# Kernel tuning notes

Hardware: AMD Instinct MI355X
Metric: run time of the kernel (lower is better)

## Reference

```python
import jax, jax.numpy as jnp
import numpy as np

NUM_EXPERTS = 8
HIDDEN = 2048
INTER = 4096
TOKENS = 8192
TOP_K = 2


def setup_inputs() -> dict:
    key = jax.random.key(0)
    ks = jax.random.split(key, 5)
    s = 0.02
    return {
        "x": jax.random.normal(ks[0], (TOKENS, HIDDEN), dtype=jnp.float32),
        "gate_w": jax.random.normal(ks[1], (NUM_EXPERTS, HIDDEN), dtype=jnp.float32) * s,
        "w1": jax.random.normal(ks[2], (NUM_EXPERTS, INTER, HIDDEN), dtype=jnp.float32) * s,
        "w2": jax.random.normal(ks[3], (NUM_EXPERTS, HIDDEN, INTER), dtype=jnp.float32) * s,
        "w3": jax.random.normal(ks[4], (NUM_EXPERTS, INTER, HIDDEN), dtype=jnp.float32) * s,
    }


def reference(x, gate_w, w1, w2, w3):
    # Router: softmax over experts in fp32, then top-2 (no renormalization,
    # matching the torch module which uses the raw top-k softmax probs).
    router_logits = jnp.einsum("th,eh->te", x, gate_w)  # [T, E]
    probs = jax.nn.softmax(router_logits.astype(jnp.float32), axis=1)
    topk_w, topk_idx = jax.lax.top_k(probs, TOP_K)  # [T, K]
    topk_w = topk_w.astype(x.dtype)

    num_experts = w1.shape[0]
    out = jnp.zeros_like(x)
    for e in range(num_experts):
        # Combined routing coefficient for expert e per token (0 if unrouted).
        coef = jnp.sum(jnp.where(topk_idx == e, topk_w, 0.0), axis=1)  # [T]
        # SwiGLU expert FFN: down(silu(gate(x)) * up(x))
        g = jnp.einsum("th,ih->ti", x, w1[e])
        u = jnp.einsum("th,ih->ti", x, w3[e])
        h = jax.nn.silu(g) * u
        y = jnp.einsum("ti,hi->th", h, w2[e])
        out = out + coef[:, None] * y
    return out
```

## Files before the change

### kernel.cpp

```cpp
#include <hip/hip_runtime.h>
#include <stdint.h>
#include <stddef.h>


constexpr int kTokens  = 8192;
constexpr int kHidden  = 2048;
constexpr int kInter   = 4096;
constexpr int kExperts = 8;

constexpr int BM = 128, BN = 128, BK = 64;
constexpr int MAX_MT = (2 * kTokens) / BM + kExperts;
constexpr int NTY = kInter / BK;
constexpr int NPAN_Y5 = kHidden / 256;
constexpr int kSlotCap = 16512;

typedef short bf16x8 __attribute__((ext_vector_type(8)));
typedef float f32x4  __attribute__((ext_vector_type(4)));
typedef unsigned int u32;

__device__ __forceinline__ unsigned short f2bf(float f) {
  union { float f; unsigned u; } v; v.f = f;
  unsigned r = v.u + 0x7FFFu + ((v.u >> 16) & 1u);
  return (unsigned short)(r >> 16);
}

__device__ __forceinline__ void gload16(const void* g, void* l) {
  __builtin_amdgcn_global_load_lds(
      (const __attribute__((address_space(1))) u32*)g,
      (__attribute__((address_space(3))) u32*)l, 16, 0, 0);
}

__global__ __launch_bounds__(256) void convert_w(
    const float* __restrict__ src, unsigned short* __restrict__ dst,
    int lp, int lq, int K, long nchunks)
{
  long stride = (long)gridDim.x * blockDim.x;
  for (long g = blockIdx.x * (long)blockDim.x + threadIdx.x; g < nchunks; g += stride) {
    int  l   = (int)(g & 1023);
    long blk = g >> 10;
    int  q   = (int)(blk & ((1 << lq) - 1));
    long ep  = blk >> lq;
    int  p   = (int)(ep & ((1 << lp) - 1));
    int  e   = (int)(ep >> lp);
    int r = l >> 3, cs = l & 7, c = cs ^ (r & 7);
    size_t soff = (((size_t)(e << lp) + p) * 128 + r) * (size_t)K + (size_t)q * 64 + c * 8;
    float4 v0 = *reinterpret_cast<const float4*>(src + soff);
    float4 v1 = *reinterpret_cast<const float4*>(src + soff + 4);
    uint4 o;
    o.x = (u32)f2bf(v0.x) | ((u32)f2bf(v0.y) << 16);
    o.y = (u32)f2bf(v0.z) | ((u32)f2bf(v0.w) << 16);
    o.z = (u32)f2bf(v1.x) | ((u32)f2bf(v1.y) << 16);
    o.w = (u32)f2bf(v1.z) | ((u32)f2bf(v1.w) << 16);
    *reinterpret_cast<uint4*>(dst + g * 8) = o;
  }
}

__global__ __launch_bounds__(256) void moe_router(
    const float* __restrict__ x, const float* __restrict__ gate_w,
    unsigned short* __restrict__ xb, int* __restrict__ counts,
    int* __restrict__ list_idx, float* __restrict__ list_w)
{
  const int lane = threadIdx.x & 63;
  const int wave = threadIdx.x >> 6;
  const int t = blockIdx.x * 4 + wave;

  float acc[kExperts];
#pragma unroll
  for (int e = 0; e < kExperts; ++e) acc[e] = 0.f;

  const float4* xrow = reinterpret_cast<const float4*>(x + (size_t)t * kHidden);
#pragma unroll
  for (int j = 0; j < 8; ++j) {
    float4 xv = xrow[j * 64 + lane];
    uint2 pk;
    pk.x = (u32)f2bf(xv.x) | ((u32)f2bf(xv.y) << 16);
    pk.y = (u32)f2bf(xv.z) | ((u32)f2bf(xv.w) << 16);
    *reinterpret_cast<uint2*>(xb + (size_t)t * kHidden + j * 256 + lane * 4) = pk;
#pragma unroll
    for (int e = 0; e < kExperts; ++e) {
      float4 gv = reinterpret_cast<const float4*>(gate_w + (size_t)e * kHidden)[j * 64 + lane];
      acc[e] += xv.x * gv.x + xv.y * gv.y + xv.z * gv.z + xv.w * gv.w;
    }
  }
#pragma unroll
  for (int e = 0; e < kExperts; ++e) {
#pragma unroll
    for (int m = 32; m >= 1; m >>= 1) acc[e] += __shfl_xor(acc[e], m);
  }
  if (lane == 0) {
    float mx = acc[0];
#pragma unroll
    for (int e = 1; e < kExperts; ++e) mx = fmaxf(mx, acc[e]);
    float p[kExperts]; float s = 0.f;
#pragma unroll
    for (int e = 0; e < kExperts; ++e) { p[e] = __expf(acc[e] - mx); s += p[e]; }
    float inv = 1.f / s;
    int i1 = 0; float v1 = p[0];
#pragma unroll
    for (int e = 1; e < kExperts; ++e) if (p[e] > v1) { v1 = p[e]; i1 = e; }
    int i2 = (i1 == 0) ? 1 : 0; float v2 = p[i2];
#pragma unroll
    for (int e = 0; e < kExperts; ++e) {
      if (e == i1 || e == i2) continue;
      if (p[e] > v2) { v2 = p[e]; i2 = e; }
    }
    int s1 = atomicAdd(&counts[i1], 1);
    list_idx[i1 * kTokens + s1] = t * 2 + 0;
    list_w [i1 * kTokens + s1] = v1 * inv;
    int s2 = atomicAdd(&counts[i2], 1);
    list_idx[i2 * kTokens + s2] = t * 2 + 1;
    list_w [i2 * kTokens + s2] = v2 * inv;
  }
}

__device__ __forceinline__ bool map_tile(const int* __restrict__ counts, int mt,
                                         int& e, int& lm, int& sb, int& ne)
{
  int tb = 0; sb = 0;
  for (e = 0; e < kExperts; ++e) {
    ne = counts[e];
    int tiles = (ne + BM - 1) / BM;
    if (mt < tb + tiles) { lm = mt - tb; return true; }
    tb += tiles; sb += ne;
  }
  return false;
}

__global__ __launch_bounds__(256, 2) void moe_gu(
    const unsigned short* __restrict__ xb,
    const unsigned short* __restrict__ w1b, const unsigned short* __restrict__ w3b,
    const int* __restrict__ counts, const int* __restrict__ list_idx,
    unsigned short* __restrict__ hbuf)
{
  __shared__ unsigned short As [BM * BK];
  __shared__ unsigned short B1s[BN * BK];
  __shared__ unsigned short B3s[BN * BK];
  __shared__ int toks[BM];

  const int tid = threadIdx.x;
  const int nt  = blockIdx.x / MAX_MT;
  const int mt  = blockIdx.x % MAX_MT;

  int e, lm, sb, ne;
  if (!map_tile(counts, mt, e, lm, sb, ne)) return;
  const int row0 = lm * BM;

  if (tid < BM) {
    int lr = row0 + tid;
    toks[tid] = list_idx[e * kTokens + ((lr < ne) ? lr : 0)] >> 1;
  }
  __syncthreads();

  const int lane = tid & 63;
  const int w = tid >> 6;
  const int wr = w >> 1, wc = w & 1;

  const unsigned short* srcA[4];
  const unsigned short* srcB1[4];
  const unsigned short* srcB3[4];
  const size_t bbase = ((size_t)(e * (kInter / BN) + nt) * (kHidden / BK)) * 1024;
#pragma unroll
  for (int i = 0; i < 4; ++i) {
    int l = (w * 4 + i) * 64 + lane;
    int r = l >> 3, cs = l & 7, c = cs ^ (r & 7);
    srcA[i]  = xb  + (size_t)toks[r] * kHidden + c * 8;
    srcB1[i] = w1b + (bbase + l) * 8;
    srcB3[i] = w3b + (bbase + l) * 8;
  }

  f32x4 accG[4][4], accU[4][4];
  const f32x4 zero = {0.f, 0.f, 0.f, 0.f};
#pragma unroll
  for (int m = 0; m < 4; ++m)
#pragma unroll
    for (int n = 0; n < 4; ++n) { accG[m][n] = zero; accU[m][n] = zero; }

  for (int ks = 0; ks < kHidden / BK; ++ks) {
#pragma unroll
    for (int i = 0; i < 4; ++i) {
      gload16(srcA[i]  + ks * BK,            &As [(w * 4 + i) * 512]);
      gload16(srcB1[i] + (size_t)ks * 8192,  &B1s[(w * 4 + i) * 512]);
      gload16(srcB3[i] + (size_t)ks * 8192,  &B3s[(w * 4 + i) * 512]);
    }
    __syncthreads();
#pragma unroll
    for (int kk = 0; kk < 2; ++kk) {
      const int cq = kk * 4 + (lane >> 4);
      bf16x8 a[4], b1v[4], b3v[4];
#pragma unroll
      for (int m = 0; m < 4; ++m) {
        int row = wr * 64 + m * 16 + (lane & 15);
        a[m] = *reinterpret_cast<const bf16x8*>(&As[row * 64 + ((cq ^ (row & 7)) << 3)]);
      }
#pragma unroll
      for (int n = 0; n < 4; ++n) {
        int row = wc * 64 + n * 16 + (lane & 15);
        b1v[n] = *reinterpret_cast<const bf16x8*>(&B1s[row * 64 + ((cq ^ (row & 7)) << 3)]);
        b3v[n] = *reinterpret_cast<const bf16x8*>(&B3s[row * 64 + ((cq ^ (row & 7)) << 3)]);
      }
#pragma unroll
      for (int m = 0; m < 4; ++m)
#pragma unroll
        for (int n = 0; n < 4; ++n) {
          accG[m][n] = __builtin_amdgcn_mfma_f32_16x16x32_bf16(a[m], b1v[n], accG[m][n], 0, 0, 0);
          accU[m][n] = __builtin_amdgcn_mfma_f32_16x16x32_bf16(a[m], b3v[n], accU[m][n], 0, 0, 0);
        }
    }
    __syncthreads();
  }

#pragma unroll
  for (int m = 0; m < 4; ++m) {
#pragma unroll
    for (int r = 0; r < 4; ++r) {
      int rloc = wr * 64 + m * 16 + ((lane >> 4) * 4) + r;
      int lrow = row0 + rloc;
      if (lrow < ne) {
        size_t base = (size_t)(sb + lrow) * kInter + (size_t)nt * BN + wc * 64 + (lane & 15);
#pragma unroll
        for (int n = 0; n < 4; ++n) {
          float g = accG[m][n][r];
          float u = accU[m][n][r];
          float hv = (g / (1.f + __expf(-g))) * u;
          hbuf[base + n * 16] = f2bf(hv);
        }
      }
    }
  }
}

__global__ __launch_bounds__(512, 4) void moe_y5(
    const unsigned short* __restrict__ hbuf,
    const unsigned short* __restrict__ w2b,
    const int* __restrict__ counts, const int* __restrict__ list_idx,
    const float* __restrict__ list_w,
    float* __restrict__ ybuf)
{
  __shared__ unsigned short As[8192];
  __shared__ unsigned short Bs[2][8192];
  __shared__ int   toks[BM];
  __shared__ float cofs[BM];
  __shared__ int   rnks[BM];

  const int tid = threadIdx.x;
  const int nt  = blockIdx.x / MAX_MT;
  const int mt  = blockIdx.x % MAX_MT;

  int e, lm, sb, ne;
  if (!map_tile(counts, mt, e, lm, sb, ne)) return;
  const int row0 = lm * BM;

  if (tid < BM) {
    int lr = row0 + tid;
    bool v = lr < ne;
    int pk = v ? list_idx[e * kTokens + lr] : 0;
    toks[tid] = pk >> 1;
    rnks[tid] = pk & 1;
    cofs[tid] = v ? list_w[e * kTokens + lr] : 0.f;
  }
  __syncthreads();

  const int lane = tid & 63;
  const int w    = tid >> 6;
  const int wr   = w >> 2;
  const int wc   = w & 3;

  const unsigned short* srcA[2];
  int cOff[2];
#pragma unroll
  for (int j = 0; j < 2; ++j) {
    int l = (w * 2 + j) * 64 + lane;
    int r = l >> 3, c = (l & 7) ^ (r & 7);
    int rg = sb + row0 + r;
    if (rg > kSlotCap - 1) rg = kSlotCap - 1;
    srcA[j] = hbuf + (size_t)rg * kInter + c * 8;
    cOff[j] = l * 8;
  }
  const unsigned short* pB[2];
#pragma unroll
  for (int h = 0; h < 2; ++h)
    pB[h] = w2b + (size_t)(e * 16 + nt * 2 + h) * NTY * 8192;

  f32x4 acc[4][4];
  const f32x4 zero = {0.f, 0.f, 0.f, 0.f};
#pragma unroll
  for (int m = 0; m < 4; ++m)
#pragma unroll
    for (int n = 0; n < 4; ++n) acc[m][n] = zero;

  for (int ks = 0; ks < NTY; ++ks) {
#pragma unroll
    for (int j = 0; j < 2; ++j) {
      gload16(srcA[j] + ks * BK, &As[(w * 2 + j) * 512]);
      gload16(pB[0] + (size_t)ks * 8192 + cOff[j], &Bs[0][(w * 2 + j) * 512]);
      gload16(pB[1] + (size_t)ks * 8192 + cOff[j], &Bs[1][(w * 2 + j) * 512]);
    }
    __syncthreads();
#pragma unroll
    for (int kk = 0; kk < 2; ++kk) {
      const int cq = kk * 4 + (lane >> 4);
      bf16x8 a[4], b[4];
#pragma unroll
      for (int m = 0; m < 4; ++m) {
        int row = wr * 64 + m * 16 + (lane & 15);
        a[m] = *reinterpret_cast<const bf16x8*>(&As[row * 64 + ((cq ^ (row & 7)) << 3)]);
      }
#pragma unroll
      for (int n = 0; n < 4; ++n) {
        int rr = wc * 64 + n * 16 + (lane & 15);
        int h = rr >> 7, rl = rr & 127;
        b[n] = *reinterpret_cast<const bf16x8*>(&Bs[h][rl * 64 + ((cq ^ (rl & 7)) << 3)]);
      }
#pragma unroll
      for (int m = 0; m < 4; ++m)
#pragma unroll
        for (int n = 0; n < 4; ++n)
          acc[m][n] = __builtin_amdgcn_mfma_f32_16x16x32_bf16(a[m], b[n], acc[m][n], 0, 0, 0);
    }
    __syncthreads();
  }

#pragma unroll
  for (int m = 0; m < 4; ++m) {
#pragma unroll
    for (int r = 0; r < 4; ++r) {
      int rloc = wr * 64 + m * 16 + ((lane >> 4) * 4) + r;
      if (row0 + rloc < ne) {
        float cf = cofs[rloc];
        size_t obase = ((size_t)rnks[rloc] * kTokens + toks[rloc]) * kHidden
                     + (size_t)nt * 256 + wc * 64 + (lane & 15);
#pragma unroll
        for (int n = 0; n < 4; ++n)
          ybuf[obase + n * 16] = cf * acc[m][n][r];
      }
    }
  }
}

__global__ __launch_bounds__(256) void moe_merge(
    const float4* __restrict__ y0, const float4* __restrict__ y1,
    float4* __restrict__ out, int n4)
{
  int stride = gridDim.x * blockDim.x;
  for (int i = blockIdx.x * blockDim.x + threadIdx.x; i < n4; i += stride) {
    float4 a = y0[i], b = y1[i];
    float4 o; o.x = a.x + b.x; o.y = a.y + b.y; o.z = a.z + b.z; o.w = a.w + b.w;
    out[i] = o;
  }
}

__global__ __launch_bounds__(256, 2) void moe_gu_f32(
    const unsigned short* __restrict__ xb,
    const float* __restrict__ w1, const float* __restrict__ w3,
    const int* __restrict__ counts, const int* __restrict__ list_idx,
    unsigned short* __restrict__ hbuf)
{
  __shared__ unsigned short As [BM * BK];
  __shared__ unsigned short B1s[BN * BK];
  __shared__ unsigned short B3s[BN * BK];
  __shared__ int toks[BM];

  const int tid = threadIdx.x;
  const int nt  = blockIdx.x / MAX_MT;
  const int mt  = blockIdx.x % MAX_MT;

  int e, lm, sb, ne;
  if (!map_tile(counts, mt, e, lm, sb, ne)) return;
  const int row0 = lm * BM;

  if (tid < BM) {
    int lr = row0 + tid;
    toks[tid] = list_idx[e * kTokens + ((lr < ne) ? lr : 0)] >> 1;
  }
  __syncthreads();

  const unsigned short* aptr[4];
#pragma unroll
  for (int i = 0; i < 4; ++i) {
    int chunk = i * 256 + tid;
    int r = chunk >> 3, c8 = chunk & 7;
    aptr[i] = xb + (size_t)toks[r] * kHidden + c8 * 8;
  }
  const float* w1e = w1 + (size_t)e * kInter * kHidden;
  const float* w3e = w3 + (size_t)e * kInter * kHidden;

  f32x4 accG[4][4], accU[4][4];
  const f32x4 zero = {0.f, 0.f, 0.f, 0.f};
#pragma unroll
  for (int m = 0; m < 4; ++m)
#pragma unroll
    for (int n = 0; n < 4; ++n) { accG[m][n] = zero; accU[m][n] = zero; }

  const int lane = tid & 63;
  const int wr = (tid >> 6) >> 1;
  const int wc = (tid >> 6) & 1;

  for (int k0 = 0; k0 < kHidden; k0 += BK) {
#pragma unroll
    for (int i = 0; i < 4; ++i) {
      int chunk = i * 256 + tid;
      uint4 v = *reinterpret_cast<const uint4*>(aptr[i] + k0);
      *reinterpret_cast<uint4*>(&As[chunk * 8]) = v;
    }
#pragma unroll
    for (int i = 0; i < 8; ++i) {
      int c = i * 256 + tid;
      int rowB = c >> 4, c16 = c & 15;
      size_t off = ((size_t)(nt * BN + rowB)) * kHidden + k0 + c16 * 4;
      float4 v1 = *reinterpret_cast<const float4*>(w1e + off);
      float4 v3 = *reinterpret_cast<const float4*>(w3e + off);
      uint2 p1, p3;
      p1.x = (u32)f2bf(v1.x) | ((u32)f2bf(v1.y) << 16);
      p1.y = (u32)f2bf(v1.z) | ((u32)f2bf(v1.w) << 16);
      p3.x = (u32)f2bf(v3.x) | ((u32)f2bf(v3.y) << 16);
      p3.y = (u32)f2bf(v3.z) | ((u32)f2bf(v3.w) << 16);
      *reinterpret_cast<uint2*>(&B1s[rowB * BK + c16 * 4]) = p1;
      *reinterpret_cast<uint2*>(&B3s[rowB * BK + c16 * 4]) = p3;
    }
    __syncthreads();
#pragma unroll
    for (int kk = 0; kk < 2; ++kk) {
      const int klo = kk * 32 + (lane >> 4) * 8;
      bf16x8 a[4], b1v[4], b3v[4];
#pragma unroll
      for (int m = 0; m < 4; ++m)
        a[m] = *reinterpret_cast<const bf16x8*>(&As[(wr * 64 + m * 16 + (lane & 15)) * BK + klo]);
#pragma unroll
      for (int n = 0; n < 4; ++n) {
        b1v[n] = *reinterpret_cast<const bf16x8*>(&B1s[(wc * 64 + n * 16 + (lane & 15)) * BK + klo]);
        b3v[n] = *reinterpret_cast<const bf16x8*>(&B3s[(wc * 64 + n * 16 + (lane & 15)) * BK + klo]);
      }
#pragma unroll
      for (int m = 0; m < 4; ++m)
#pragma unroll
        for (int n = 0; n < 4; ++n) {
          accG[m][n] = __builtin_amdgcn_mfma_f32_16x16x32_bf16(a[m], b1v[n], accG[m][n], 0, 0, 0);
          accU[m][n] = __builtin_amdgcn_mfma_f32_16x16x32_bf16(a[m], b3v[n], accU[m][n], 0, 0, 0);
        }
    }
    __syncthreads();
  }
#pragma unroll
  for (int m = 0; m < 4; ++m) {
#pragma unroll
    for (int r = 0; r < 4; ++r) {
      int rloc = wr * 64 + m * 16 + ((lane >> 4) * 4) + r;
      int lrow = row0 + rloc;
      if (lrow < ne) {
        size_t base = (size_t)(sb + lrow) * kInter + (size_t)nt * BN + wc * 64 + (lane & 15);
#pragma unroll
        for (int n = 0; n < 4; ++n) {
          float g = accG[m][n][r];
          float u = accU[m][n][r];
          hbuf[base + n * 16] = f2bf((g / (1.f + __expf(-g))) * u);
        }
      }
    }
  }
}

__global__ __launch_bounds__(256, 2) void moe_y_f32(
    const unsigned short* __restrict__ hbuf,
    const float* __restrict__ w2,
    const int* __restrict__ counts, const int* __restrict__ list_idx,
    const float* __restrict__ list_w,
    float* __restrict__ out)
{
  __shared__ unsigned short As[BM * BK];
  __shared__ unsigned short Bs[BN * BK];
  __shared__ int   toks[BM];
  __shared__ float cofs[BM];

  const int tid = threadIdx.x;
  const int nt  = blockIdx.x / MAX_MT;
  const int mt  = blockIdx.x % MAX_MT;

  int e, lm, sb, ne;
  if (!map_tile(counts, mt, e, lm, sb, ne)) return;
  const int row0 = lm * BM;

  if (tid < BM) {
    int lr = row0 + tid;
    bool v = lr < ne;
    toks[tid] = v ? (list_idx[e * kTokens + lr] >> 1) : 0;
    cofs[tid] = v ? list_w [e * kTokens + lr] : 0.f;
  }
  __syncthreads();

  const float* w2e = w2 + (size_t)e * kHidden * kInter;
  const unsigned short* arow = hbuf + (size_t)(sb + row0) * kInter;

  f32x4 acc[4][4];
  const f32x4 zero = {0.f, 0.f, 0.f, 0.f};
#pragma unroll
  for (int m = 0; m < 4; ++m)
#pragma unroll
    for (int n = 0; n < 4; ++n) acc[m][n] = zero;

  const int lane = tid & 63;
  const int wr = (tid >> 6) >> 1;
  const int wc = (tid >> 6) & 1;

  for (int k0 = 0; k0 < kInter; k0 += BK) {
#pragma unroll
    for (int i = 0; i < 4; ++i) {
      int chunk = i * 256 + tid;
      int r = chunk >> 3, c8 = chunk & 7;
      uint4 v = *reinterpret_cast<const uint4*>(arow + (size_t)r * kInter + k0 + c8 * 8);
      *reinterpret_cast<uint4*>(&As[chunk * 8]) = v;
    }
#pragma unroll
    for (int i = 0; i < 8; ++i) {
      int c = i * 256 + tid;
      int rowB = c >> 4, c16 = c & 15;
      size_t off = ((size_t)(nt * BN + rowB)) * kInter + k0 + c16 * 4;
      float4 v2 = *reinterpret_cast<const float4*>(w2e + off);
      uint2 p2;
      p2.x = (u32)f2bf(v2.x) | ((u32)f2bf(v2.y) << 16);
      p2.y = (u32)f2bf(v2.z) | ((u32)f2bf(v2.w) << 16);
      *reinterpret_cast<uint2*>(&Bs[rowB * BK + c16 * 4]) = p2;
    }
    __syncthreads();
#pragma unroll
    for (int kk = 0; kk < 2; ++kk) {
      const int klo = kk * 32 + (lane >> 4) * 8;
      bf16x8 a[4], b[4];
#pragma unroll
      for (int m = 0; m < 4; ++m)
        a[m] = *reinterpret_cast<const bf16x8*>(&As[(wr * 64 + m * 16 + (lane & 15)) * BK + klo]);
#pragma unroll
      for (int n = 0; n < 4; ++n)
        b[n] = *reinterpret_cast<const bf16x8*>(&Bs[(wc * 64 + n * 16 + (lane & 15)) * BK + klo]);
#pragma unroll
      for (int m = 0; m < 4; ++m)
#pragma unroll
        for (int n = 0; n < 4; ++n)
          acc[m][n] = __builtin_amdgcn_mfma_f32_16x16x32_bf16(a[m], b[n], acc[m][n], 0, 0, 0);
    }
    __syncthreads();
  }
#pragma unroll
  for (int m = 0; m < 4; ++m) {
#pragma unroll
    for (int r = 0; r < 4; ++r) {
      int rloc = wr * 64 + m * 16 + ((lane >> 4) * 4) + r;
      if (row0 + rloc < ne) {
        float cf = cofs[rloc];
        size_t obase = (size_t)toks[rloc] * kHidden + (size_t)nt * BN + wc * 64 + (lane & 15);
#pragma unroll
        for (int n = 0; n < 4; ++n)
          atomicAdd(&out[obase + n * 16], cf * acc[m][n][r]);
      }
    }
  }
}

extern "C" void kernel_launch(void* const* d_in, const int* in_sizes, int n_in,
                              void* d_out, int out_size, void* d_ws, size_t ws_size,
                              hipStream_t stream)
{
  const float* x      = (const float*)d_in[0];
  const float* gate_w = (const float*)d_in[1];
  const float* w1     = (const float*)d_in[2];
  const float* w2     = (const float*)d_in[3];
  const float* w3     = (const float*)d_in[4];
  float* out = (float*)d_out;

  char* ws = (char*)d_ws;
  const size_t MiB = 1ull << 20;
  int*   counts   = (int*)(ws);
  int*   list_idx = (int*)(ws + 1024);
  float* list_w   = (float*)(ws + 1024 + kExperts * kTokens * 4);

  hipMemsetAsync(counts, 0, 1024, stream);

  if (ws_size >= 418 * MiB) {
    unsigned short* xb   = (unsigned short*)(ws + 1 * MiB);
    unsigned short* w1b  = (unsigned short*)(ws + 33 * MiB);
    unsigned short* w3b  = (unsigned short*)(ws + 161 * MiB);
    unsigned short* hbuf = (unsigned short*)(ws + 289 * MiB);
    unsigned short* w2b  = w1b;
    float*          ybuf = (float*)(ws + 161 * MiB);

    const long nch = (long)kExperts * 32 * 32 * 1024;
    convert_w<<<4096, 256, 0, stream>>>(w1, w1b, 5, 5, kHidden, nch);
    convert_w<<<4096, 256, 0, stream>>>(w3, w3b, 5, 5, kHidden, nch);
    moe_router<<<kTokens / 4, 256, 0, stream>>>(x, gate_w, xb, counts, list_idx, list_w);
    moe_gu<<<(kInter / BN) * MAX_MT, 256, 0, stream>>>(xb, w1b, w3b, counts, list_idx, hbuf);
    convert_w<<<4096, 256, 0, stream>>>(w2, w2b, 4, 6, kInter, nch);
    moe_y5<<<NPAN_Y5 * MAX_MT, 512, 0, stream>>>(hbuf, w2b, counts, list_idx, list_w, ybuf);
    moe_merge<<<2048, 256, 0, stream>>>(
        (const float4*)ybuf, (const float4*)(ybuf + (size_t)kTokens * kHidden),
        (float4*)out, kTokens * kHidden / 4);
  } else {
    unsigned short* xb   = (unsigned short*)(ws + 1 * MiB);
    unsigned short* hbuf = (unsigned short*)(ws + 36 * MiB);
    hipMemsetAsync(out, 0, (size_t)kTokens * kHidden * sizeof(float), stream);
    moe_router<<<kTokens / 4, 256, 0, stream>>>(x, gate_w, xb, counts, list_idx, list_w);
    moe_gu_f32<<<(kInter / BN) * MAX_MT, 256, 0, stream>>>(xb, w1, w3, counts, list_idx, hbuf);
    moe_y_f32 <<<(kHidden / BN) * MAX_MT, 256, 0, stream>>>(hbuf, w2, counts, list_idx, list_w, out);
  }
}
```

Measured before the change: 1.444 ms.

## Fuse router with weight conversion, split-K down GEMM, store bf16 partials

Merges the router and the w1/w3 fp32-to-bf16 conversions into one launch with block-range dispatch, so the small router work overlaps the conversion. The down-projection is split across two K halves with twice as many blocks, raising parallelism for the GEMM. Partial outputs are now written as bf16 into four buffers and summed by a new merge kernel, which halves partial-output bandwidth but adds bf16 rounding of partial sums. Launch bounds for the down GEMM drop from 4 to 2 blocks per CU.

```diff
diff --git a/kernel.cpp b/kernel.cpp
--- a/kernel.cpp
+++ b/kernel.cpp
@@ -11,7 +11,6 @@
 constexpr int BM = 128, BN = 128, BK = 64;
 constexpr int MAX_MT = (2 * kTokens) / BM + kExperts;
 constexpr int NTY = kInter / BK;
-constexpr int NPAN_Y5 = kHidden / 256;
 constexpr int kSlotCap = 16512;
 
 typedef short bf16x8 __attribute__((ext_vector_type(8)));
@@ -30,12 +29,12 @@
       (__attribute__((address_space(3))) u32*)l, 16, 0, 0);
 }
 
-__global__ __launch_bounds__(256) void convert_w(
+__device__ __forceinline__ void convert_body(
     const float* __restrict__ src, unsigned short* __restrict__ dst,
-    int lp, int lq, int K, long nchunks)
-{
-  long stride = (long)gridDim.x * blockDim.x;
-  for (long g = blockIdx.x * (long)blockDim.x + threadIdx.x; g < nchunks; g += stride) {
+    int lp, int lq, int K, long nchunks, int bid, int nblocks)
+{
+  long stride = (long)nblocks * 256;
+  for (long g = bid * 256L + threadIdx.x; g < nchunks; g += stride) {
     int  l   = (int)(g & 1023);
     long blk = g >> 10;
     int  q   = (int)(blk & ((1 << lq) - 1));
@@ -55,14 +54,21 @@
   }
 }
 
-__global__ __launch_bounds__(256) void moe_router(
+__global__ __launch_bounds__(256) void convert_w(
+    const float* __restrict__ src, unsigned short* __restrict__ dst,
+    int lp, int lq, int K, long nchunks)
+{
+  convert_body(src, dst, lp, lq, K, nchunks, blockIdx.x, gridDim.x);
+}
+
+__device__ __forceinline__ void router_body(
     const float* __restrict__ x, const float* __restrict__ gate_w,
     unsigned short* __restrict__ xb, int* __restrict__ counts,
-    int* __restrict__ list_idx, float* __restrict__ list_w)
+    int* __restrict__ list_idx, float* __restrict__ list_w, int bid)
 {
   const int lane = threadIdx.x & 63;
   const int wave = threadIdx.x >> 6;
-  const int t = blockIdx.x * 4 + wave;
+  const int t = bid * 4 + wave;
 
   float acc[kExperts];
 #pragma unroll
@@ -113,6 +119,32 @@
   }
 }
 
+__global__ __launch_bounds__(256) void moe_prep(
+    const float* __restrict__ x, const float* __restrict__ gate_w,
+    unsigned short* __restrict__ xb, int* __restrict__ counts,
+    int* __restrict__ list_idx, float* __restrict__ list_w,
+    const float* __restrict__ w1, unsigned short* __restrict__ w1b,
+    const float* __restrict__ w3, unsigned short* __restrict__ w3b,
+    long nchunks)
+{
+  const int bid = blockIdx.x;
+  if (bid < 2048) {
+    router_body(x, gate_w, xb, counts, list_idx, list_w, bid);
+  } else if (bid < 2048 + 4096) {
+    convert_body(w1, w1b, 5, 5, kHidden, nchunks, bid - 2048, 4096);
+  } else {
+    convert_body(w3, w3b, 5, 5, kHidden, nchunks, bid - 6144, 4096);
+  }
+}
+
+__global__ __launch_bounds__(256) void moe_router(
+    const float* __restrict__ x, const float* __restrict__ gate_w,
+    unsigned short* __restrict__ xb, int* __restrict__ counts,
+    int* __restrict__ list_idx, float* __restrict__ list_w)
+{
+  router_body(x, gate_w, xb, counts, list_idx, list_w, blockIdx.x);
+}
+
 __device__ __forceinline__ bool map_tile(const int* __restrict__ counts, int mt,
                                          int& e, int& lm, int& sb, int& ne)
 {
@@ -229,12 +261,12 @@
   }
 }
 
-__global__ __launch_bounds__(512, 4) void moe_y5(
+__global__ __launch_bounds__(512, 2) void moe_y8(
     const unsigned short* __restrict__ hbuf,
     const unsigned short* __restrict__ w2b,
     const int* __restrict__ counts, const int* __restrict__ list_idx,
     const float* __restrict__ list_w,
-    float* __restrict__ ybuf)
+    unsigned short* __restrict__ ybuf16)
 {
   __shared__ unsigned short As[8192];
   __shared__ unsigned short Bs[2][8192];
@@ -243,8 +275,10 @@
   __shared__ int   rnks[BM];
 
   const int tid = threadIdx.x;
-  const int nt  = blockIdx.x / MAX_MT;
+  const int grp = blockIdx.x / MAX_MT;
   const int mt  = blockIdx.x % MAX_MT;
+  const int ks  = grp >> 3;
+  const int nt  = grp & 7;
 
   int e, lm, sb, ne;
   if (!map_tile(counts, mt, e, lm, sb, ne)) return;
@@ -288,12 +322,13 @@
 #pragma unroll
     for (int n = 0; n < 4; ++n) acc[m][n] = zero;
 
-  for (int ks = 0; ks < NTY; ++ks) {
+  const int kt0 = ks * (NTY / 2);
+  for (int kt = kt0; kt < kt0 + NTY / 2; ++kt) {
 #pragma unroll
     for (int j = 0; j < 2; ++j) {
-      gload16(srcA[j] + ks * BK, &As[(w * 2 + j) * 512]);
-      gload16(pB[0] + (size_t)ks * 8192 + cOff[j], &Bs[0][(w * 2 + j) * 512]);
-      gload16(pB[1] + (size_t)ks * 8192 + cOff[j], &Bs[1][(w * 2 + j) * 512]);
+      gload16(srcA[j] + kt * BK, &As[(w * 2 + j) * 512]);
+      gload16(pB[0] + (size_t)kt * 8192 + cOff[j], &Bs[0][(w * 2 + j) * 512]);
+      gload16(pB[1] + (size_t)kt * 8192 + cOff[j], &Bs[1][(w * 2 + j) * 512]);
     }
     __syncthreads();
 #pragma unroll
@@ -327,25 +362,39 @@
       int rloc = wr * 64 + m * 16 + ((lane >> 4) * 4) + r;
       if (row0 + rloc < ne) {
         float cf = cofs[rloc];
-        size_t obase = ((size_t)rnks[rloc] * kTokens + toks[rloc]) * kHidden
+        size_t obase = ((size_t)(rnks[rloc] * 2 + ks) * kTokens + toks[rloc]) * kHidden
                      + (size_t)nt * 256 + wc * 64 + (lane & 15);
 #pragma unroll
         for (int n = 0; n < 4; ++n)
-          ybuf[obase + n * 16] = cf * acc[m][n][r];
-      }
-    }
-  }
-}
-
-__global__ __launch_bounds__(256) void moe_merge(
-    const float4* __restrict__ y0, const float4* __restrict__ y1,
-    float4* __restrict__ out, int n4)
-{
-  int stride = gridDim.x * blockDim.x;
-  for (int i = blockIdx.x * blockDim.x + threadIdx.x; i < n4; i += stride) {
-    float4 a = y0[i], b = y1[i];
-    float4 o; o.x = a.x + b.x; o.y = a.y + b.y; o.z = a.z + b.z; o.w = a.w + b.w;
-    out[i] = o;
+          ybuf16[obase + n * 16] = f2bf(cf * acc[m][n][r]);
+      }
+    }
+  }
+}
+
+__global__ __launch_bounds__(256) void moe_merge4(
+    const unsigned short* __restrict__ yb, float* __restrict__ out, long n8)
+{
+  const size_t bs = (size_t)kTokens * kHidden;
+  long stride = (long)gridDim.x * blockDim.x;
+  for (long i = blockIdx.x * (long)blockDim.x + threadIdx.x; i < n8; i += stride) {
+    float s[8];
+#pragma unroll
+    for (int k = 0; k < 8; ++k) s[k] = 0.f;
+#pragma unroll
+    for (int b = 0; b < 4; ++b) {
+      uint4 v = *reinterpret_cast<const uint4*>(yb + b * bs + (size_t)i * 8);
+      const unsigned short* h = reinterpret_cast<const unsigned short*>(&v);
+#pragma unroll
+      for (int k = 0; k < 8; ++k) {
+        union { unsigned u; float f; } cv; cv.u = (unsigned)h[k] << 16;
+        s[k] += cv.f;
+      }
+    }
+    float4 o0 = {s[0], s[1], s[2], s[3]};
+    float4 o1 = {s[4], s[5], s[6], s[7]};
+    *reinterpret_cast<float4*>(out + (size_t)i * 8)     = o0;
+    *reinterpret_cast<float4*>(out + (size_t)i * 8 + 4) = o1;
   }
 }
 
@@ -575,23 +624,20 @@
   hipMemsetAsync(counts, 0, 1024, stream);
 
   if (ws_size >= 418 * MiB) {
-    unsigned short* xb   = (unsigned short*)(ws + 1 * MiB);
-    unsigned short* w1b  = (unsigned short*)(ws + 33 * MiB);
-    unsigned short* w3b  = (unsigned short*)(ws + 161 * MiB);
-    unsigned short* hbuf = (unsigned short*)(ws + 289 * MiB);
-    unsigned short* w2b  = w1b;
-    float*          ybuf = (float*)(ws + 161 * MiB);
+    unsigned short* xb     = (unsigned short*)(ws + 1 * MiB);
+    unsigned short* w1b    = (unsigned short*)(ws + 33 * MiB);
+    unsigned short* w3b    = (unsigned short*)(ws + 161 * MiB);
+    unsigned short* hbuf   = (unsigned short*)(ws + 289 * MiB);
+    unsigned short* w2b    = w1b;
+    unsigned short* ybuf16 = (unsigned short*)(ws + 161 * MiB);
 
     const long nch = (long)kExperts * 32 * 32 * 1024;
-    convert_w<<<4096, 256, 0, stream>>>(w1, w1b, 5, 5, kHidden, nch);
-    convert_w<<<4096, 256, 0, stream>>>(w3, w3b, 5, 5, kHidden, nch);
-    moe_router<<<kTokens / 4, 256, 0, stream>>>(x, gate_w, xb, counts, list_idx, list_w);
+    moe_prep<<<10240, 256, 0, stream>>>(x, gate_w, xb, counts, list_idx, list_w,
+                                        w1, w1b, w3, w3b, nch);
     moe_gu<<<(kInter / BN) * MAX_MT, 256, 0, stream>>>(xb, w1b, w3b, counts, list_idx, hbuf);
     convert_w<<<4096, 256, 0, stream>>>(w2, w2b, 4, 6, kInter, nch);
-    moe_y5<<<NPAN_Y5 * MAX_MT, 512, 0, stream>>>(hbuf, w2b, counts, list_idx, list_w, ybuf);
-    moe_merge<<<2048, 256, 0, stream>>>(
-        (const float4*)ybuf, (const float4*)(ybuf + (size_t)kTokens * kHidden),
-        (float4*)out, kTokens * kHidden / 4);
+    moe_y8<<<16 * MAX_MT, 512, 0, stream>>>(hbuf, w2b, counts, list_idx, list_w, ybuf16);
+    moe_merge4<<<2048, 256, 0, stream>>>(ybuf16, out, (long)kTokens * kHidden / 8);
   } else {
     unsigned short* xb   = (unsigned short*)(ws + 1 * MiB);
     unsigned short* hbuf = (unsigned short*)(ws + 36 * MiB);
```

Measured after the change: 1.410 ms. -2.4%, faster.
